# Performance work log

Hardware: AMD Instinct MI355X
Metric: run time of the kernel (lower is better)

## Reference

```python
import jax, jax.numpy as jnp
import numpy as np

NUM_CLASSES = 100
NUM_PROTOS = 10
FEAT_DIM = 1024
BATCH = 16384
NALL = NUM_CLASSES * NUM_PROTOS


def setup_inputs() -> dict:
    key = jax.random.key(0)
    k1, k2, k3 = jax.random.split(key, 3)
    x = jax.random.normal(k1, (BATCH, FEAT_DIM), dtype=jnp.float32)
    protos = jax.random.normal(k2, (NALL, FEAT_DIM), dtype=jnp.float32)
    enc_w = jax.random.normal(k3, (FEAT_DIM, FEAT_DIM), dtype=jnp.float32) / np.sqrt(FEAT_DIM)
    enc_b = jnp.zeros((FEAT_DIM,), dtype=jnp.float32)
    return {"x": x, "protos": protos, "enc_w": enc_w, "enc_b": enc_b}


def reference(x, protos, enc_w, enc_b):
    # encoder(protos): linear projection, (nall, F)
    ep = protos @ enc_w + enc_b
    # Pairwise euclidean distance via GEMM-based squared-distance trick:
    x_sq = jnp.sum(x * x, axis=-1, keepdims=True)            # (B, 1)
    p_sq = jnp.sum(ep * ep, axis=-1)                          # (nall,)
    d2 = x_sq - 2.0 * (x @ ep.T) + p_sq[None, :]              # (B, nall)
    d = jnp.sqrt(jnp.maximum(d2, 0.0))                        # L2 norm, clamp fp error
    # reshape matches torch: index = proto * num_classes + class
    d = d.reshape(x.shape[0], NUM_PROTOS, NUM_CLASSES)
    return jnp.min(d, axis=1)                                 # (B, num_classes)
```

## Files before the change

kernel.cpp:

```cpp
#include <hip/hip_runtime.h>
#include <hip/hip_bf16.h>
#include <stdint.h>

#define FEAT 1024
#define NALL 1000
#define NPAD 1120
#define NCLS 100
#define LDSBUF 28672

typedef __attribute__((ext_vector_type(8))) short short8;
typedef __attribute__((ext_vector_type(4))) float f32x4;
typedef __attribute__((ext_vector_type(4))) unsigned short us4;

__device__ __forceinline__ unsigned short f2bf(float f) {
    union { float f; uint32_t u; } v; v.f = f;
    uint32_t u = v.u;
    return (unsigned short)((u + 0x7FFFu + ((u >> 16) & 1u)) >> 16);
}

__device__ __forceinline__ void gload16(const void* g, void* l) {
    __builtin_amdgcn_global_load_lds((__attribute__((address_space(1))) void*)g,
                                     (__attribute__((address_space(3))) void*)l,
                                     16, 0, 0);
}

__global__ __launch_bounds__(256) void k_prep_x(const float* __restrict__ x,
                                                unsigned short* __restrict__ xb,
                                                float* __restrict__ xsq) {
    int row = blockIdx.x * 4 + (threadIdx.x >> 6);
    int lane = threadIdx.x & 63;
    const float4* xr = (const float4*)(x + (size_t)row * FEAT);
    float s = 0.f;
#pragma unroll
    for (int i = 0; i < 4; ++i) {
        float4 v = xr[lane + i * 64];
        s += v.x * v.x + v.y * v.y + v.z * v.z + v.w * v.w;
        us4 o;
        o[0] = f2bf(v.x); o[1] = f2bf(v.y); o[2] = f2bf(v.z); o[3] = f2bf(v.w);
        *(us4*)(xb + (size_t)row * FEAT + (size_t)(lane + i * 64) * 4) = o;
    }
#pragma unroll
    for (int off = 32; off; off >>= 1) s += __shfl_xor(s, off);
    if (lane == 0) xsq[row] = s;
}

__global__ __launch_bounds__(256) void k_prep_protos(const float* __restrict__ p,
                                                     unsigned short* __restrict__ pb) {
    int row = blockIdx.x;
    int t = threadIdx.x;
    us4 o;
    if (row < NALL) {
        float4 v = ((const float4*)(p + (size_t)row * FEAT))[t];
        o[0] = f2bf(v.x); o[1] = f2bf(v.y); o[2] = f2bf(v.z); o[3] = f2bf(v.w);
    } else {
        o[0] = 0; o[1] = 0; o[2] = 0; o[3] = 0;
    }
    *(us4*)(pb + (size_t)row * FEAT + (size_t)t * 4) = o;
}

__global__ __launch_bounds__(256) void k_transpose_w(const float* __restrict__ w,
                                                     unsigned short* __restrict__ wt) {
    __shared__ float tile[32][33];
    int bx = blockIdx.x, by = blockIdx.y;
    int tx = threadIdx.x & 31, ty = threadIdx.x >> 5;
#pragma unroll
    for (int i = 0; i < 4; ++i) {
        int r = by * 32 + ty + i * 8;
        tile[ty + i * 8][tx] = w[(size_t)r * FEAT + bx * 32 + tx];
    }
    __syncthreads();
#pragma unroll
    for (int i = 0; i < 4; ++i) {
        int r = bx * 32 + ty + i * 8;
        wt[(size_t)r * FEAT + by * 32 + tx] = f2bf(tile[tx][ty + i * 8]);
    }
}

__global__ __launch_bounds__(256) void k_enc_gemm(const unsigned short* __restrict__ A,
                                                  const unsigned short* __restrict__ B,
                                                  const float* __restrict__ bias,
                                                  unsigned short* __restrict__ epb) {
    __shared__ __align__(16) char smem[32768];
    int bm0 = (blockIdx.x >> 3) * 128;
    int bn0 = (blockIdx.x & 7) * 128;
    int tid = threadIdx.x, lane = tid & 63, wid = tid >> 6;
    int wm = wid >> 1, wn = wid & 1;
    int ls = lane >> 4, lf = lane & 15;
    f32x4 acc[4][4] = {};
    for (int k0 = 0; k0 < FEAT; k0 += 64) {
        __syncthreads();
#pragma unroll
        for (int i = 0; i < 4; ++i) {
            int ci = wid + i * 4;
            int r = ci * 8 + (lane >> 3), c = (lane & 7) * 8;
            gload16(A + (size_t)(bm0 + r) * FEAT + k0 + c, smem + ci * 1024);
            gload16(B + (size_t)(bn0 + r) * FEAT + k0 + c, smem + 16384 + ci * 1024);
        }
        __syncthreads();
#pragma unroll
        for (int kk = 0; kk < 64; kk += 32) {
            short8 a[4], b[4];
#pragma unroll
            for (int f = 0; f < 4; ++f) {
                a[f] = *(const short8*)(smem + (wm * 64 + f * 16 + lf) * 128 + (kk + ls * 8) * 2);
                b[f] = *(const short8*)(smem + 16384 + (wn * 64 + f * 16 + lf) * 128 + (kk + ls * 8) * 2);
            }
#pragma unroll
            for (int fm = 0; fm < 4; ++fm)
#pragma unroll
                for (int fn = 0; fn < 4; ++fn)
                    acc[fm][fn] = __builtin_amdgcn_mfma_f32_16x16x32_bf16(a[fm], b[fn], acc[fm][fn], 0, 0, 0);
        }
    }
    int tr = ls * 4, tc = lf;
#pragma unroll
    for (int fn = 0; fn < 4; ++fn) {
        int col = bn0 + wn * 64 + fn * 16 + tc;
        float bb = bias[col];
#pragma unroll
        for (int fm = 0; fm < 4; ++fm) {
#pragma unroll
            for (int r = 0; r < 4; ++r) {
                int row = bm0 + wm * 64 + fm * 16 + tr + r;
                if (row < NALL) {
                    int pr = (row % 100) * 10 + row / 100;
                    epb[(size_t)pr * FEAT + col] = f2bf(acc[fm][fn][r] + bb);
                }
            }
        }
    }
}

__global__ __launch_bounds__(256) void k_psq(const unsigned short* __restrict__ epb,
                                             float* __restrict__ psq) {
    int row = blockIdx.x * 4 + (threadIdx.x >> 6);
    int lane = threadIdx.x & 63;
    if (row >= NPAD) return;
    float s = 0.f;
    const short8* r8 = (const short8*)(epb + (size_t)row * FEAT);
#pragma unroll
    for (int i = 0; i < 2; ++i) {
        short8 v = r8[lane + i * 64];
#pragma unroll
        for (int j = 0; j < 8; ++j) {
            union { uint32_t u; float f; } c;
            c.u = ((uint32_t)(unsigned short)v[j]) << 16;
            s += c.f * c.f;
        }
    }
#pragma unroll
    for (int off = 32; off; off >>= 1) s += __shfl_xor(s, off);
    if (lane == 0) psq[row] = (row < NALL) ? s : 1e30f;
}

__global__ __launch_bounds__(512) void k_main(const unsigned short* __restrict__ xb,
                                              const unsigned short* __restrict__ epb,
                                              const float* __restrict__ xsq,
                                              const float* __restrict__ psq,
                                              float* __restrict__ out) {
    __shared__ __align__(16) char smem[116352];
    const int bid = blockIdx.x;
    const int swz = (bid & 7) * 56 + (bid >> 3);
    const int bm0 = (swz / 7) * 256;
    const int bn0 = (swz % 7) * 160;
    const int tid = threadIdx.x, lane = tid & 63, wid = tid >> 6;
    const int wm = wid >> 1, wn = wid & 1;
    const int ls = lane >> 4, lf = lane & 15;
    float* xsq_s = (float*)(smem + 114688);
    float* psq_s = (float*)(smem + 115712);
    if (tid < 256) xsq_s[tid] = xsq[bm0 + tid];
    if (tid < 160) psq_s[tid] = psq[bn0 + tid];

    const int sr  = lane >> 2;
    const int scb = (lane & 3) ^ ((lane >> 3) & 3);
    const unsigned short* sp[4];
    int ldo[4];
    if (wid < 4) {
#pragma unroll
        for (int i = 0; i < 4; ++i) {
            int ci = wid + i * 4;
            sp[i]  = xb + (size_t)(bm0 + ci * 16 + sr) * FEAT + scb * 8;
            ldo[i] = ci * 1024;
        }
    } else {
#pragma unroll
        for (int i = 0; i < 3; ++i) {
            int ci = (wid - 4) + i * 4;
            sp[i]  = epb + (size_t)(bn0 + ci * 16 + sr) * FEAT + scb * 8;
            ldo[i] = 16384 + ci * 1024;
        }
        sp[3] = nullptr; ldo[3] = 0;
    }

#define STAGE(S) do {                                                          \
    char* bb_ = smem + ((S) & 3) * LDSBUF;                                     \
    if (wid < 4) {                                                             \
        _Pragma("unroll")                                                      \
        for (int i_ = 0; i_ < 4; ++i_)                                         \
            gload16(sp[i_] + (S) * 32, bb_ + ldo[i_]);                         \
    } else {                                                                   \
        _Pragma("unroll")                                                      \
        for (int i_ = 0; i_ < 3; ++i_)                                         \
            gload16(sp[i_] + (S) * 32, bb_ + ldo[i_]);                         \
    }                                                                          \
} while (0)

    const int sw2 = (lf >> 1) & 3;
    const int off = ((ls ^ sw2) << 4);
    int raA[4], raB[5];
#pragma unroll
    for (int f = 0; f < 4; ++f) raA[f] = (wm * 64 + f * 16 + lf) * 64 + off;
#pragma unroll
    for (int f = 0; f < 5; ++f) raB[f] = 16384 + (wn * 80 + f * 16 + lf) * 64 + off;

    f32x4 acc[4][5] = {};

    STAGE(0); STAGE(1); STAGE(2);
    if (wid < 4) asm volatile("s_waitcnt vmcnt(8)" ::: "memory");
    else         asm volatile("s_waitcnt vmcnt(6)" ::: "memory");
    __builtin_amdgcn_s_barrier();

#pragma unroll
    for (int s = 0; s < 32; ++s) {
        const char* base = (const char*)smem + (s & 3) * LDSBUF;
        short8 a[4], b[5];
#pragma unroll
        for (int f = 0; f < 4; ++f) a[f] = *(const short8*)(base + raA[f]);
#pragma unroll
        for (int f = 0; f < 5; ++f) b[f] = *(const short8*)(base + raB[f]);
        if (s + 3 < 32) STAGE(s + 3);
        if (s <= 28) {
            if (wid < 4) asm volatile("s_waitcnt vmcnt(8)" ::: "memory");
            else         asm volatile("s_waitcnt vmcnt(6)" ::: "memory");
        } else if (s == 29) {
            if (wid < 4) asm volatile("s_waitcnt vmcnt(4)" ::: "memory");
            else         asm volatile("s_waitcnt vmcnt(3)" ::: "memory");
        } else if (s == 30) {
            asm volatile("s_waitcnt vmcnt(0)" ::: "memory");
        }
        __builtin_amdgcn_s_setprio(1);
#pragma unroll
        for (int fm = 0; fm < 4; ++fm)
#pragma unroll
            for (int fn = 0; fn < 5; ++fn)
                acc[fm][fn] = __builtin_amdgcn_mfma_f32_16x16x32_bf16(a[fm], b[fn], acc[fm][fn], 0, 0, 0);
        __builtin_amdgcn_s_setprio(0);
        __builtin_amdgcn_s_barrier();
    }
#undef STAGE

    float* dls = (float*)smem;
    const int tr = ls * 4;
    const int cls0 = bn0 / 10;
#pragma unroll
    for (int p = 0; p < 4; ++p) {
#pragma unroll
        for (int fn = 0; fn < 5; ++fn) {
            int col = wn * 80 + fn * 16 + lf;
            float pq = psq_s[col];
#pragma unroll
            for (int r = 0; r < 4; ++r) {
                float d2 = xsq_s[wm * 64 + p * 16 + tr + r] - 2.f * acc[p][fn][r] + pq;
                dls[(wm * 16 + tr + r) * 161 + col] = sqrtf(fmaxf(d2, 0.f));
            }
        }
        __syncthreads();
#pragma unroll
        for (int i = 0; i < 2; ++i) {
            int task = tid + i * 512;
            int rr = task >> 4, cl = task & 15;
            float m = 1e30f;
#pragma unroll
            for (int j = 0; j < 10; ++j) m = fminf(m, dls[rr * 161 + cl * 10 + j]);
            int grow = bm0 + (rr >> 4) * 64 + p * 16 + (rr & 15);
            int gcls = cls0 + cl;
            if (gcls < NCLS) out[(size_t)grow * NCLS + gcls] = m;
        }
        if (p < 3) __syncthreads();
    }
}

extern "C" void kernel_launch(void* const* d_in, const int* in_sizes, int n_in,
                              void* d_out, int out_size, void* d_ws, size_t ws_size,
                              hipStream_t stream) {
    const float* x      = (const float*)d_in[0];
    const float* protos = (const float*)d_in[1];
    const float* enc_w  = (const float*)d_in[2];
    const float* enc_b  = (const float*)d_in[3];
    float* out = (float*)d_out;
    char* ws = (char*)d_ws;

    unsigned short* xb  = (unsigned short*)ws;
    unsigned short* epb = (unsigned short*)(ws + 33554432);
    unsigned short* prb = (unsigned short*)(ws + 35913728);
    unsigned short* wtb = (unsigned short*)(ws + 38010880);
    float* xsq = (float*)(ws + 40108032);
    float* psq = (float*)(ws + 40173568);

    hipMemsetAsync(epb + (size_t)1000 * FEAT, 0, (size_t)152 * FEAT * 2, stream);

    k_prep_x<<<4096, 256, 0, stream>>>(x, xb, xsq);
    k_prep_protos<<<1024, 256, 0, stream>>>(protos, prb);
    k_transpose_w<<<dim3(32, 32), 256, 0, stream>>>(enc_w, wtb);
    k_enc_gemm<<<64, 256, 0, stream>>>(prb, wtb, enc_b, epb);
    k_psq<<<280, 256, 0, stream>>>(epb, psq);
    k_main<<<448, 512, 0, stream>>>(xb, epb, xsq, psq, out);
}
```

Before: 112.3 us.

## Widen main GEMM tile to 256x320 with overlapping last column block

The main distance kernel's N tile is doubled from 160 to 320 prototype columns, so the grid shrinks from 448 to 256 blocks. The last column block starts at 800 and overlaps the previous one, so recomputed columns are written redundantly instead of padding N to 1280. Each wave now holds 4x10 accumulators and reads B from LDS more often per A load, which raises arithmetic intensity per staged byte. The pipeline also gains a barrier before the MFMA phase, plus sched_barriers to pin instruction order. This raises register pressure and LDS use (about 146 KB), and with only 256 blocks on 256 CUs there is one wave of work with no tail to hide.

Measured after the change: 158.2 us. 40.8% more time.

```diff
diff --git a/kernel.cpp b/kernel.cpp
--- a/kernel.cpp
+++ b/kernel.cpp
@@ -6,7 +6,7 @@
 #define NALL 1000
 #define NPAD 1120
 #define NCLS 100
-#define LDSBUF 28672
+#define LB 36864
 
 typedef __attribute__((ext_vector_type(8))) short short8;
 typedef __attribute__((ext_vector_type(4))) float f32x4;
@@ -153,28 +153,31 @@
     if (lane == 0) psq[row] = (row < NALL) ? s : 1e30f;
 }
 
-__global__ __launch_bounds__(512) void k_main(const unsigned short* __restrict__ xb,
-                                              const unsigned short* __restrict__ epb,
-                                              const float* __restrict__ xsq,
-                                              const float* __restrict__ psq,
-                                              float* __restrict__ out) {
-    __shared__ __align__(16) char smem[116352];
+#define WAITV(n) asm volatile("s_waitcnt vmcnt(" #n ")")
+
+__global__ __launch_bounds__(512, 2) void k_main(const unsigned short* __restrict__ xb,
+                                                 const unsigned short* __restrict__ epb,
+                                                 const float* __restrict__ xsq,
+                                                 const float* __restrict__ psq,
+                                                 float* __restrict__ out) {
+    __shared__ __align__(16) char smem[149760];
     const int bid = blockIdx.x;
-    const int swz = (bid & 7) * 56 + (bid >> 3);
-    const int bm0 = (swz / 7) * 256;
-    const int bn0 = (swz % 7) * 160;
+    const int xcd = bid & 7, loc = bid >> 3;
+    const int bm0 = (xcd * 8 + (loc >> 2)) * 256;
+    const int nb  = loc & 3;
+    const int bn0 = (nb == 3) ? 800 : nb * 320;
     const int tid = threadIdx.x, lane = tid & 63, wid = tid >> 6;
     const int wm = wid >> 1, wn = wid & 1;
     const int ls = lane >> 4, lf = lane & 15;
-    float* xsq_s = (float*)(smem + 114688);
-    float* psq_s = (float*)(smem + 115712);
+    float* xsq_s = (float*)(smem + 147456);
+    float* psq_s = (float*)(smem + 148480);
     if (tid < 256) xsq_s[tid] = xsq[bm0 + tid];
-    if (tid < 160) psq_s[tid] = psq[bn0 + tid];
+    if (tid < 320) psq_s[tid] = psq[bn0 + tid];
 
     const int sr  = lane >> 2;
     const int scb = (lane & 3) ^ ((lane >> 3) & 3);
-    const unsigned short* sp[4];
-    int ldo[4];
+    const unsigned short* sp[5];
+    int ldo[5];
     if (wid < 4) {
 #pragma unroll
         for (int i = 0; i < 4; ++i) {
@@ -182,69 +185,73 @@
             sp[i]  = xb + (size_t)(bm0 + ci * 16 + sr) * FEAT + scb * 8;
             ldo[i] = ci * 1024;
         }
+        sp[4] = nullptr; ldo[4] = 0;
     } else {
 #pragma unroll
-        for (int i = 0; i < 3; ++i) {
+        for (int i = 0; i < 5; ++i) {
             int ci = (wid - 4) + i * 4;
             sp[i]  = epb + (size_t)(bn0 + ci * 16 + sr) * FEAT + scb * 8;
             ldo[i] = 16384 + ci * 1024;
         }
-        sp[3] = nullptr; ldo[3] = 0;
     }
 
 #define STAGE(S) do {                                                          \
-    char* bb_ = smem + ((S) & 3) * LDSBUF;                                     \
+    char* bb_ = smem + ((S) & 3) * LB;                                         \
     if (wid < 4) {                                                             \
         _Pragma("unroll")                                                      \
         for (int i_ = 0; i_ < 4; ++i_)                                         \
             gload16(sp[i_] + (S) * 32, bb_ + ldo[i_]);                         \
     } else {                                                                   \
         _Pragma("unroll")                                                      \
-        for (int i_ = 0; i_ < 3; ++i_)                                         \
+        for (int i_ = 0; i_ < 5; ++i_)                                         \
             gload16(sp[i_] + (S) * 32, bb_ + ldo[i_]);                         \
     }                                                                          \
 } while (0)
 
-    const int sw2 = (lf >> 1) & 3;
-    const int off = ((ls ^ sw2) << 4);
-    int raA[4], raB[5];
-#pragma unroll
-    for (int f = 0; f < 4; ++f) raA[f] = (wm * 64 + f * 16 + lf) * 64 + off;
-#pragma unroll
-    for (int f = 0; f < 5; ++f) raB[f] = 16384 + (wn * 80 + f * 16 + lf) * 64 + off;
-
-    f32x4 acc[4][5] = {};
+    const int off = ((ls ^ ((lf >> 1) & 3)) << 4);
+    int raA[4], raB[10];
+#pragma unroll
+    for (int f = 0; f < 4; ++f)  raA[f] = (wm * 64 + f * 16 + lf) * 64 + off;
+#pragma unroll
+    for (int f = 0; f < 10; ++f) raB[f] = 16384 + (wn * 160 + f * 16 + lf) * 64 + off;
+
+    f32x4 acc[4][10] = {};
 
     STAGE(0); STAGE(1); STAGE(2);
-    if (wid < 4) asm volatile("s_waitcnt vmcnt(8)" ::: "memory");
-    else         asm volatile("s_waitcnt vmcnt(6)" ::: "memory");
+    __builtin_amdgcn_sched_barrier(0);
+    if (wid < 4) WAITV(8); else WAITV(10);
+    __builtin_amdgcn_sched_barrier(0);
     __builtin_amdgcn_s_barrier();
+    __builtin_amdgcn_sched_barrier(0);
 
 #pragma unroll
     for (int s = 0; s < 32; ++s) {
-        const char* base = (const char*)smem + (s & 3) * LDSBUF;
-        short8 a[4], b[5];
-#pragma unroll
-        for (int f = 0; f < 4; ++f) a[f] = *(const short8*)(base + raA[f]);
-#pragma unroll
-        for (int f = 0; f < 5; ++f) b[f] = *(const short8*)(base + raB[f]);
+        const char* base = (const char*)smem + (s & 3) * LB;
+        short8 a[4], b[10];
+#pragma unroll
+        for (int f = 0; f < 4; ++f)  a[f] = *(const short8*)(base + raA[f]);
+#pragma unroll
+        for (int f = 0; f < 10; ++f) b[f] = *(const short8*)(base + raB[f]);
         if (s + 3 < 32) STAGE(s + 3);
+        __builtin_amdgcn_sched_barrier(0);
         if (s <= 28) {
-            if (wid < 4) asm volatile("s_waitcnt vmcnt(8)" ::: "memory");
-            else         asm volatile("s_waitcnt vmcnt(6)" ::: "memory");
+            if (wid < 4) WAITV(8); else WAITV(10);
         } else if (s == 29) {
-            if (wid < 4) asm volatile("s_waitcnt vmcnt(4)" ::: "memory");
-            else         asm volatile("s_waitcnt vmcnt(3)" ::: "memory");
+            if (wid < 4) WAITV(4); else WAITV(5);
         } else if (s == 30) {
-            asm volatile("s_waitcnt vmcnt(0)" ::: "memory");
-        }
+            WAITV(0);
+        }
+        __builtin_amdgcn_sched_barrier(0);
+        __builtin_amdgcn_s_barrier();
+        __builtin_amdgcn_sched_barrier(0);
         __builtin_amdgcn_s_setprio(1);
 #pragma unroll
         for (int fm = 0; fm < 4; ++fm)
 #pragma unroll
-            for (int fn = 0; fn < 5; ++fn)
+            for (int fn = 0; fn < 10; ++fn)
                 acc[fm][fn] = __builtin_amdgcn_mfma_f32_16x16x32_bf16(a[fm], b[fn], acc[fm][fn], 0, 0, 0);
         __builtin_amdgcn_s_setprio(0);
+        __builtin_amdgcn_sched_barrier(0);
         __builtin_amdgcn_s_barrier();
     }
 #undef STAGE
@@ -255,23 +262,23 @@
 #pragma unroll
     for (int p = 0; p < 4; ++p) {
 #pragma unroll
-        for (int fn = 0; fn < 5; ++fn) {
-            int col = wn * 80 + fn * 16 + lf;
+        for (int fn = 0; fn < 10; ++fn) {
+            int col = wn * 160 + fn * 16 + lf;
             float pq = psq_s[col];
 #pragma unroll
             for (int r = 0; r < 4; ++r) {
                 float d2 = xsq_s[wm * 64 + p * 16 + tr + r] - 2.f * acc[p][fn][r] + pq;
-                dls[(wm * 16 + tr + r) * 161 + col] = sqrtf(fmaxf(d2, 0.f));
+                dls[(wm * 16 + tr + r) * 321 + col] = sqrtf(fmaxf(d2, 0.f));
             }
         }
         __syncthreads();
 #pragma unroll
-        for (int i = 0; i < 2; ++i) {
+        for (int i = 0; i < 4; ++i) {
             int task = tid + i * 512;
-            int rr = task >> 4, cl = task & 15;
+            int rr = task >> 5, cl = task & 31;
             float m = 1e30f;
 #pragma unroll
-            for (int j = 0; j < 10; ++j) m = fminf(m, dls[rr * 161 + cl * 10 + j]);
+            for (int j = 0; j < 10; ++j) m = fminf(m, dls[rr * 321 + cl * 10 + j]);
             int grow = bm0 + (rr >> 4) * 64 + p * 16 + (rr & 15);
             int gcls = cls0 + cl;
             if (gcls < NCLS) out[(size_t)grow * NCLS + gcls] = m;
@@ -292,17 +299,17 @@
 
     unsigned short* xb  = (unsigned short*)ws;
     unsigned short* epb = (unsigned short*)(ws + 33554432);
-    unsigned short* prb = (unsigned short*)(ws + 35913728);
-    unsigned short* wtb = (unsigned short*)(ws + 38010880);
-    float* xsq = (float*)(ws + 40108032);
-    float* psq = (float*)(ws + 40173568);
-
-    hipMemsetAsync(epb + (size_t)1000 * FEAT, 0, (size_t)152 * FEAT * 2, stream);
+    unsigned short* prb = (unsigned short*)(ws + 35848192);
+    unsigned short* wtb = (unsigned short*)(ws + 37945344);
+    float* xsq = (float*)(ws + 40042496);
+    float* psq = (float*)(ws + 40108032);
+
+    hipMemsetAsync(epb + (size_t)1000 * FEAT, 0, (size_t)120 * FEAT * 2, stream);
 
     k_prep_x<<<4096, 256, 0, stream>>>(x, xb, xsq);
     k_prep_protos<<<1024, 256, 0, stream>>>(protos, prb);
     k_transpose_w<<<dim3(32, 32), 256, 0, stream>>>(enc_w, wtb);
     k_enc_gemm<<<64, 256, 0, stream>>>(prb, wtb, enc_b, epb);
     k_psq<<<280, 256, 0, stream>>>(epb, psq);
-    k_main<<<448, 512, 0, stream>>>(xb, epb, xsq, psq, out);
-}
+    k_main<<<256, 512, 0, stream>>>(xb, epb, xsq, psq, out);
+}
```
